# Kernel tuning notes

Measured on AMD Instinct MI355X. Metric: run time of the kernel, lower is better.

## Reference

```python
import jax, jax.numpy as jnp
import numpy as np
import math

N_HEADS = 16
EMBED_DIM = 1024
HEAD_DIM = EMBED_DIM // N_HEADS


def setup_inputs() -> dict:
    key = jax.random.key(0)
    k1, k2, k3 = jax.random.split(key, 3)
    bs, seq_len = 2, 2048
    x = jax.random.normal(k1, (bs, seq_len, EMBED_DIM), dtype=jnp.float32)
    # torch Linear weights are [out_features, in_features]
    W_in = jax.random.normal(k2, (3 * EMBED_DIM, EMBED_DIM), dtype=jnp.float32) * (1.0 / math.sqrt(EMBED_DIM))
    W_out = jax.random.normal(k3, (EMBED_DIM, EMBED_DIM), dtype=jnp.float32) * (1.0 / math.sqrt(EMBED_DIM))
    return {"x": x, "W_in": W_in, "W_out": W_out, "casual_mask": 1}


def reference(x, W_in, W_out, casual_mask):
    bs, seq_len, embed_dim = x.shape
    # fused QKV projection: x @ W_in.T -> [bs, seq, 3E]
    qkv = jnp.einsum('bse,fe->bsf', x, W_in)
    q, k, v = jnp.split(qkv, 3, axis=-1)
    # [bs, heads, seq, head_dim]
    def to_heads(t):
        return t.reshape(bs, seq_len, N_HEADS, HEAD_DIM).transpose(0, 2, 1, 3)
    q, k, v = to_heads(q), to_heads(k), to_heads(v)
    score = jnp.einsum('bhqd,bhkd->bhqk', q, k)
    if casual_mask:  # static Python flag
        causal = jnp.triu(jnp.ones((seq_len, seq_len), dtype=bool), k=1)
        score = jnp.where(causal, -jnp.inf, score)
    score = score / jnp.asarray(math.sqrt(HEAD_DIM), dtype=score.dtype)
    attn = jax.nn.softmax(score, axis=-1)
    out = jnp.einsum('bhqk,bhkd->bhqd', attn, v)
    out = out.transpose(0, 2, 1, 3).reshape(bs, seq_len, embed_dim)
    return jnp.einsum('bse,fe->bsf', out, W_out)
```

## Files before the change

kernel.cpp:

```cpp
#include <hip/hip_runtime.h>
#include <stdint.h>

#define SEQ 2048
#define BS 2
#define EMB 1024
#define NH 16
#define HD 64
#define F3 3072

using f32x4 = __attribute__((ext_vector_type(4))) float;
using bf16x8 = __attribute__((ext_vector_type(8))) short;

__device__ __forceinline__ unsigned short f2bf(float f) {
    union { float f; uint32_t u; } v; v.f = f;
    uint32_t u = v.u;
    u = u + 0x7FFFu + ((u >> 16) & 1u);
    return (unsigned short)(u >> 16);
}

__device__ __forceinline__ uint32_t pk_bf16(float a, float b) {
    uint32_t r;
    asm("v_cvt_pk_bf16_f32 %0, %1, %2" : "=v"(r) : "v"(a), "v"(b));
    return r;
}

#define GLOAD_LDS16(g, l) \
    __builtin_amdgcn_global_load_lds((const __attribute__((address_space(1))) void*)(g), \
                                     (__attribute__((address_space(3))) void*)(l), 16, 0, 0)

__global__ void cvt_kernel(const float* __restrict__ in, unsigned short* __restrict__ out, int n4) {
    int i = blockIdx.x * blockDim.x + threadIdx.x;
    if (i < n4) {
        f32x4 v = reinterpret_cast<const f32x4*>(in)[i];
        uint2 o;
        o.x = pk_bf16(v.x, v.y);
        o.y = pk_bf16(v.z, v.w);
        reinterpret_cast<uint2*>(out)[i] = o;
    }
}

template <bool QKV>
__global__ __launch_bounds__(256) void gemm_bt(
    const unsigned short* __restrict__ A,
    const unsigned short* __restrict__ B,
    void* __restrict__ Cv,
    unsigned short* __restrict__ vT,
    int M, int N, int K, int nbx)
{
    __shared__ unsigned short As[2][128 * 32];
    __shared__ unsigned short Bs[2][128 * 32];
    const int tid  = threadIdx.x;
    const int wave = tid >> 6, lane = tid & 63;
    const int wr = wave >> 1, wc = wave & 1;

    const int nwg = gridDim.x;
    const int sw = (blockIdx.x & 7) * (nwg >> 3) + (blockIdx.x >> 3);
    const int bx = sw % nbx, by = sw / nbx;
    const int row0 = by * 128, col0 = bx * 128;

    f32x4 acc[4][4] = {};

    const int srow = wave * 16 + (lane >> 2);
    const int scol = (lane & 3) * 8;

    const unsigned short* gA = A + (size_t)(row0 + srow) * K + scol;
    const unsigned short* gB = B + (size_t)(col0 + srow) * K + scol;
    const int lofs = wave * 16 * 32;

#define STAGE_G(buf, kb) do { \
    GLOAD_LDS16(gA + (kb),                   As[buf] + lofs); \
    GLOAD_LDS16(gA + (size_t)64 * K + (kb),  As[buf] + 64 * 32 + lofs); \
    GLOAD_LDS16(gB + (kb),                   Bs[buf] + lofs); \
    GLOAD_LDS16(gB + (size_t)64 * K + (kb),  Bs[buf] + 64 * 32 + lofs); } while (0)

    STAGE_G(0, 0);
    asm volatile("s_waitcnt vmcnt(0)" ::: "memory");
    __syncthreads();

    int cur = 0;
    for (int kb = 0; kb < K; kb += 32) {
        if (kb + 32 < K) STAGE_G(cur ^ 1, kb + 32);

        bf16x8 af[4], bfr[4];
#pragma unroll
        for (int mi = 0; mi < 4; mi++)
            af[mi] = *reinterpret_cast<const bf16x8*>(As[cur] + (wr * 64 + mi * 16 + (lane & 15)) * 32 + (lane >> 4) * 8);
#pragma unroll
        for (int ni = 0; ni < 4; ni++)
            bfr[ni] = *reinterpret_cast<const bf16x8*>(Bs[cur] + (wc * 64 + ni * 16 + (lane & 15)) * 32 + (lane >> 4) * 8);
#pragma unroll
        for (int mi = 0; mi < 4; mi++)
#pragma unroll
            for (int ni = 0; ni < 4; ni++)
                acc[mi][ni] = __builtin_amdgcn_mfma_f32_16x16x32_bf16(af[mi], bfr[ni], acc[mi][ni], 0, 0, 0);

        asm volatile("s_waitcnt vmcnt(0)" ::: "memory");
        __syncthreads();
        cur ^= 1;
    }
#undef STAGE_G

    if constexpr (QKV) {
        if (col0 >= 2 * EMB) {
#pragma unroll
            for (int mi = 0; mi < 4; mi++)
#pragma unroll
                for (int ni = 0; ni < 4; ni++) {
                    int vcol = col0 - 2 * EMB + wc * 64 + ni * 16 + (lane & 15);
                    int hh = vcol >> 6, dd = vcol & 63;
                    int row = row0 + wr * 64 + mi * 16 + (lane >> 4) * 4;
                    int bb = row >> 11, ss = row & 2047;
                    uint2 pk;
                    pk.x = pk_bf16(acc[mi][ni][0], acc[mi][ni][1]);
                    pk.y = pk_bf16(acc[mi][ni][2], acc[mi][ni][3]);
                    *reinterpret_cast<uint2*>(vT + (size_t)((bb * 16 + hh) * 64 + dd) * 2048 + ss) = pk;
                }
        } else {
#pragma unroll
            for (int mi = 0; mi < 4; mi++)
#pragma unroll
                for (int ni = 0; ni < 4; ni++)
#pragma unroll
                    for (int r = 0; r < 4; r++) {
                        int row = row0 + wr * 64 + mi * 16 + (lane >> 4) * 4 + r;
                        int col = col0 + wc * 64 + ni * 16 + (lane & 15);
                        ((unsigned short*)Cv)[(size_t)row * N + col] = f2bf(acc[mi][ni][r]);
                    }
        }
    } else {
#pragma unroll
        for (int mi = 0; mi < 4; mi++)
#pragma unroll
            for (int ni = 0; ni < 4; ni++)
#pragma unroll
                for (int r = 0; r < 4; r++) {
                    int row = row0 + wr * 64 + mi * 16 + (lane >> 4) * 4 + r;
                    int col = col0 + wc * 64 + ni * 16 + (lane & 15);
                    ((float*)Cv)[(size_t)row * N + col] = acc[mi][ni][r];
                }
    }
}

__global__ __launch_bounds__(256) void attn_kernel(
    const unsigned short* __restrict__ qkv,
    const unsigned short* __restrict__ vT,
    unsigned short* __restrict__ ao)
{
    const int o = blockIdx.x;
    const int pos = o >> 3;
    const int bh = (o & 7) * 4 + (pos & 3);
    const int qb = 31 - (pos >> 2);
    const int b = bh >> 4, h = bh & 15;
    const int tid = threadIdx.x, wave = tid >> 6, lane = tid & 63;
    const int c = lane & 15, g = lane >> 4;

    __shared__ unsigned short Ks[64 * 64];
    __shared__ unsigned short Vs[64 * 64];
    __shared__ unsigned short Ps[4][16 * 64];

    const size_t base = (size_t)b * SEQ * F3;
    const int qrow0 = qb * 64 + wave * 16;
    const float SC = 0.18033688011f;

    bf16x8 qf[2];
#pragma unroll
    for (int sdq = 0; sdq < 2; sdq++) {
        int row = qrow0 + c;
        int d   = sdq * 32 + g * 8;
        qf[sdq] = *reinterpret_cast<const bf16x8*>(qkv + base + (size_t)row * F3 + h * HD + d);
    }

    f32x4 po[4] = {};
    float mR = -1e30f, lR = 0.f;

    const int ktiles = qb + 1;
    const int vrow = tid >> 3;
    const int sch  = tid & 7;

    const unsigned short* gK  = qkv + base + EMB + h * HD + sch * 8;
    const unsigned short* gVT = vT + (size_t)bh * 64 * SEQ + sch * 8;

    bf16x8 kp0 = *reinterpret_cast<const bf16x8*>(gK + (size_t)vrow * F3);
    bf16x8 kp1 = *reinterpret_cast<const bf16x8*>(gK + (size_t)(32 + vrow) * F3);
    bf16x8 vp0 = *reinterpret_cast<const bf16x8*>(gVT + (size_t)vrow * SEQ);
    bf16x8 vp1 = *reinterpret_cast<const bf16x8*>(gVT + (size_t)(32 + vrow) * SEQ);

    for (int kt_i = 0; kt_i < ktiles; kt_i++) {
        const int kbase = kt_i * 64;
        __syncthreads();
        {
            int off0 = (vrow * 128 + sch * 16) ^ ((vrow & 7) << 4);
            *reinterpret_cast<bf16x8*>((char*)Ks + off0) = kp0;
            int r1 = 32 + vrow;
            int off1 = (r1 * 128 + sch * 16) ^ ((r1 & 7) << 4);
            *reinterpret_cast<bf16x8*>((char*)Ks + off1) = kp1;
            int vo0 = (vrow * 128 + sch * 16) ^ ((((vrow & 7) ^ (vrow >> 3)) & 7) << 4);
            *reinterpret_cast<bf16x8*>((char*)Vs + vo0) = vp0;
            int vo1 = (r1 * 128 + sch * 16) ^ ((((r1 & 7) ^ (r1 >> 3)) & 7) << 4);
            *reinterpret_cast<bf16x8*>((char*)Vs + vo1) = vp1;
        }
        __syncthreads();

        if (kt_i + 1 < ktiles) {
            const int nb = kbase + 64;
            kp0 = *reinterpret_cast<const bf16x8*>(gK + (size_t)(nb + vrow) * F3);
            kp1 = *reinterpret_cast<const bf16x8*>(gK + (size_t)(nb + 32 + vrow) * F3);
            vp0 = *reinterpret_cast<const bf16x8*>(gVT + (size_t)vrow * SEQ + nb);
            vp1 = *reinterpret_cast<const bf16x8*>(gVT + (size_t)(32 + vrow) * SEQ + nb);
        }

        f32x4 st[4] = {};
#pragma unroll
        for (int dstep = 0; dstep < 2; dstep++) {
            bf16x8 kf[4];
#pragma unroll
            for (int kt = 0; kt < 4; kt++) {
                int row = kt * 16 + c;
                int off = (row * 128 + dstep * 64 + g * 16) ^ ((row & 7) << 4);
                kf[kt] = *reinterpret_cast<const bf16x8*>((char*)Ks + off);
            }
#pragma unroll
            for (int kt = 0; kt < 4; kt++)
                st[kt] = __builtin_amdgcn_mfma_f32_16x16x32_bf16(kf[kt], qf[dstep], st[kt], 0, 0, 0);
        }

        const bool needmask = (kt_i == qb);
        {
            const int q = qrow0 + c;
            float mx = -3.0e38f;
#pragma unroll
            for (int kt = 0; kt < 4; kt++)
#pragma unroll
                for (int r = 0; r < 4; r++) {
                    float v = st[kt][r];
                    if (needmask) {
                        int k = kbase + kt * 16 + g * 4 + r;
                        if (k > q) v = -3.0e38f;
                    }
                    st[kt][r] = v;
                    mx = fmaxf(mx, v);
                }
            mx = fmaxf(mx, __shfl_xor(mx, 16));
            mx = fmaxf(mx, __shfl_xor(mx, 32));

            const bool skip = __all(mx - mR <= 8.0f);
            float mn = skip ? mR : fmaxf(mR, mx);
            const float nmn = -mn * SC;
            float rs = 0.f;
#pragma unroll
            for (int kt = 0; kt < 4; kt++)
#pragma unroll
                for (int r = 0; r < 4; r++) {
                    float p = __builtin_amdgcn_exp2f(__builtin_fmaf(st[kt][r], SC, nmn));
                    st[kt][r] = p;
                    rs += p;
                }
            rs += __shfl_xor(rs, 16);
            rs += __shfl_xor(rs, 32);
            if (skip) {
                lR += rs;
            } else {
                float alpha = __builtin_amdgcn_exp2f((mR - mn) * SC);
                mR = mn;
                lR = lR * alpha + rs;
#pragma unroll
                for (int r = 0; r < 4; r++) {
                    float ar = __shfl(alpha, (g << 2) + r);
#pragma unroll
                    for (int ni = 0; ni < 4; ni++) po[ni][r] *= ar;
                }
            }
        }

        unsigned short* Pw = Ps[wave];
        {
#pragma unroll
            for (int kt = 0; kt < 4; kt++) {
                uint2 pk;
                pk.x = pk_bf16(st[kt][0], st[kt][1]);
                pk.y = pk_bf16(st[kt][2], st[kt][3]);
                int off = (c * 128 + kt * 32 + g * 8) ^ ((c & 7) << 4);
                *reinterpret_cast<uint2*>((char*)Pw + off) = pk;
            }
        }

#pragma unroll
        for (int s2 = 0; s2 < 2; s2++) {
            bf16x8 pa, vb[4];
            {
                int off = (c * 128 + s2 * 64 + g * 16) ^ ((c & 7) << 4);
                pa = *reinterpret_cast<const bf16x8*>((char*)Pw + off);
            }
#pragma unroll
            for (int ni = 0; ni < 4; ni++) {
                int n = ni * 16 + c;
                int off = (n * 128 + s2 * 64 + g * 16) ^ ((((n & 7) ^ (n >> 3)) & 7) << 4);
                vb[ni] = *reinterpret_cast<const bf16x8*>((char*)Vs + off);
            }
#pragma unroll
            for (int ni = 0; ni < 4; ni++)
                po[ni] = __builtin_amdgcn_mfma_f32_16x16x32_bf16(pa, vb[ni], po[ni], 0, 0, 0);
        }
    }

    {
        float invl = 1.0f / lR;
#pragma unroll
        for (int r = 0; r < 4; r++) {
            float iv = __shfl(invl, (g << 2) + r);
            int row = qrow0 + g * 4 + r;
#pragma unroll
            for (int ni = 0; ni < 4; ni++) {
                int d = ni * 16 + c;
                ao[(size_t)(b * SEQ + row) * EMB + h * HD + d] = f2bf(po[ni][r] * iv);
            }
        }
    }
}

extern "C" void kernel_launch(void* const* d_in, const int* in_sizes, int n_in,
                              void* d_out, int out_size, void* d_ws, size_t ws_size,
                              hipStream_t stream)
{
    const float* x    = (const float*)d_in[0];
    const float* Win  = (const float*)d_in[1];
    const float* Wout = (const float*)d_in[2];
    float* out = (float*)d_out;

    char* ws = (char*)d_ws;
    unsigned short* xb    = (unsigned short*)(ws);
    unsigned short* winb  = (unsigned short*)(ws + (8u  << 20));
    unsigned short* woutb = (unsigned short*)(ws + (14u << 20));
    unsigned short* qkvb  = (unsigned short*)(ws + (16u << 20));
    unsigned short* aob   = (unsigned short*)(ws + (40u << 20));
    unsigned short* vtb   = (unsigned short*)(ws + (48u << 20));

    const int nx    = BS * SEQ * EMB;
    const int nwin  = F3 * EMB;
    const int nwout = EMB * EMB;

    cvt_kernel<<<nx    / 4 / 256, 256, 0, stream>>>(x,    xb,    nx / 4);
    cvt_kernel<<<nwin  / 4 / 256, 256, 0, stream>>>(Win,  winb,  nwin / 4);
    cvt_kernel<<<nwout / 4 / 256, 256, 0, stream>>>(Wout, woutb, nwout / 4);

    gemm_bt<true><<<dim3(768), 256, 0, stream>>>(xb, winb, (void*)qkvb, vtb, BS * SEQ, F3, EMB, F3 / 128);

    attn_kernel<<<dim3(1024), 256, 0, stream>>>(qkvb, vtb, aob);

    gemm_bt<false><<<dim3(256), 256, 0, stream>>>(aob, woutb, (void*)out, nullptr, BS * SEQ, EMB, EMB, EMB / 128);
}
```

Before: 180.6 us.

## Merge bf16 conversion launches, rebalance causal attention block order, prioritise MFMA waves

The three fp32-to-bf16 conversion launches become one kernel that picks its source by index and writes into the contiguous bf16 workspace. The causal attention grid is remapped so that consecutive groups of blocks take query tiles m, 15-m, 16+m and 31-m. The aim is to give each compute unit a similar total amount of masked work, replacing the previous heavy-first order. s_setprio is raised around the QK and PV MFMA loops so matrix waves get issue priority over softmax and load waves. The single conversion launch relies on xb, winb and woutb being adjacent in the workspace, and the balancing relies on the hardware dispatching blocks round-robin.

```diff
diff --git a/kernel.cpp b/kernel.cpp
--- a/kernel.cpp
+++ b/kernel.cpp
@@ -28,15 +28,21 @@
     __builtin_amdgcn_global_load_lds((const __attribute__((address_space(1))) void*)(g), \
                                      (__attribute__((address_space(3))) void*)(l), 16, 0, 0)
 
-__global__ void cvt_kernel(const float* __restrict__ in, unsigned short* __restrict__ out, int n4) {
+__global__ void cvt_kernel(const float* __restrict__ x, const float* __restrict__ win,
+                           const float* __restrict__ wout, unsigned short* __restrict__ outb) {
+    const int NX4 = BS * SEQ * EMB / 4;
+    const int NW4 = NX4 + F3 * EMB / 4;
     int i = blockIdx.x * blockDim.x + threadIdx.x;
-    if (i < n4) {
-        f32x4 v = reinterpret_cast<const f32x4*>(in)[i];
-        uint2 o;
-        o.x = pk_bf16(v.x, v.y);
-        o.y = pk_bf16(v.z, v.w);
-        reinterpret_cast<uint2*>(out)[i] = o;
-    }
+    const float* src;
+    int j;
+    if (i < NX4)       { src = x;    j = i; }
+    else if (i < NW4)  { src = win;  j = i - NX4; }
+    else               { src = wout; j = i - NW4; }
+    f32x4 v = reinterpret_cast<const f32x4*>(src)[j];
+    uint2 o;
+    o.x = pk_bf16(v.x, v.y);
+    o.y = pk_bf16(v.z, v.w);
+    reinterpret_cast<uint2*>(outb)[i] = o;
 }
 
 template <bool QKV>
@@ -147,9 +153,10 @@
     unsigned short* __restrict__ ao)
 {
     const int o = blockIdx.x;
-    const int pos = o >> 3;
-    const int bh = (o & 7) * 4 + (pos & 3);
-    const int qb = 31 - (pos >> 2);
+    const int bh = o & 31;
+    const int m_ = (o >> 5) & 7;
+    const int r_ = o >> 8;
+    const int qb = (r_ == 0) ? m_ : (r_ == 1) ? 15 - m_ : (r_ == 2) ? 16 + m_ : 31 - m_;
     const int b = bh >> 4, h = bh & 15;
     const int tid = threadIdx.x, wave = tid >> 6, lane = tid & 63;
     const int c = lane & 15, g = lane >> 4;
@@ -210,6 +217,7 @@
         }
 
         f32x4 st[4] = {};
+        __builtin_amdgcn_s_setprio(1);
 #pragma unroll
         for (int dstep = 0; dstep < 2; dstep++) {
             bf16x8 kf[4];
@@ -223,6 +231,7 @@
             for (int kt = 0; kt < 4; kt++)
                 st[kt] = __builtin_amdgcn_mfma_f32_16x16x32_bf16(kf[kt], qf[dstep], st[kt], 0, 0, 0);
         }
+        __builtin_amdgcn_s_setprio(0);
 
         const bool needmask = (kt_i == qb);
         {
@@ -284,6 +293,7 @@
             }
         }
 
+        __builtin_amdgcn_s_setprio(1);
 #pragma unroll
         for (int s2 = 0; s2 < 2; s2++) {
             bf16x8 pa, vb[4];
@@ -301,6 +311,7 @@
             for (int ni = 0; ni < 4; ni++)
                 po[ni] = __builtin_amdgcn_mfma_f32_16x16x32_bf16(pa, vb[ni], po[ni], 0, 0, 0);
         }
+        __builtin_amdgcn_s_setprio(0);
     }
 
     {
@@ -335,13 +346,7 @@
     unsigned short* aob   = (unsigned short*)(ws + (40u << 20));
     unsigned short* vtb   = (unsigned short*)(ws + (48u << 20));
 
-    const int nx    = BS * SEQ * EMB;
-    const int nwin  = F3 * EMB;
-    const int nwout = EMB * EMB;
-
-    cvt_kernel<<<nx    / 4 / 256, 256, 0, stream>>>(x,    xb,    nx / 4);
-    cvt_kernel<<<nwin  / 4 / 256, 256, 0, stream>>>(Win,  winb,  nwin / 4);
-    cvt_kernel<<<nwout / 4 / 256, 256, 0, stream>>>(Wout, woutb, nwout / 4);
+    cvt_kernel<<<dim3(8192), 256, 0, stream>>>(x, Win, Wout, xb);
 
     gemm_bt<true><<<dim3(768), 256, 0, stream>>>(xb, winb, (void*)qkvb, vtb, BS * SEQ, F3, EMB, F3 / 128);
 
```

New measurement: 180.4 us. Within noise of the previous version (-0.1%).
